# Kernel optimization log

Hardware: AMD Instinct MI355X
Metric: run time of the kernel (lower is better)

## Reference

```python
import math
import jax, jax.numpy as jnp
import numpy as np

# Neuron / simulation constants (from docstring defaults)
THETA = 10.0
TAU_SR = 10.0
TAU_REF = 1.0
SCALE_REF = 2.0
SCALE_RHO = 1.0
TS = 1.0
T_SAMPLE = 300


def _alpha_kernel(tau, mult, eps_tol):
    # Faithful to slayer._calculateAlphaKernel: eps(t) = mult * t/tau * exp(1 - t/tau),
    # truncated once |eps| < eps_tol and t > tau.
    vals = []
    for t in np.arange(0.0, T_SAMPLE, TS):
        v = mult * t / tau * math.exp(1.0 - t / tau)
        if abs(v) < eps_tol and t > tau:
            break
        vals.append(v)
    return np.asarray(vals, np.float32)


def psp(spike, srm_kernel):
    # slayerCuda.conv: causal temporal convolution psp[t] = sum_k f[k] * spike[t-k]
    N, C, H, W, T = spike.shape
    x = spike.reshape(-1, 1, T)                       # (B,1,T), B = N*C*H*W
    K = srm_kernel.shape[0]
    w = jnp.flip(srm_kernel).reshape(1, 1, K).astype(x.dtype)
    y = jax.lax.conv_general_dilated(
        x, w, window_strides=(1,), padding=[(K - 1, 0)],
        dimension_numbers=('NCH', 'OIH', 'NCH'))
    return y.reshape(N, C, H, W, T)


def get_spikes(u2, ref_kernel):
    # slayerCuda.getSpikes: sequential scan over time. At each step the effective
    # membrane potential is u[t] plus pending refractory contributions from past
    # spikes; a spike (value 1/Ts) fires when u_eff >= theta and injects the
    # refractory kernel into future timesteps.
    # u2: (B, T); ref_kernel: (K,) with ref_kernel[0] == 0 (alpha kernel).
    B, T = u2.shape
    K = ref_kernel.shape[0]
    ref_tail = ref_kernel[1:].astype(u2.dtype)        # contributions to t+1..t+K-1

    def step(pend, u_t):
        u_eff = u_t + pend[:, 0]
        s = (u_eff >= THETA).astype(u2.dtype)
        pend = jnp.concatenate([pend[:, 1:], jnp.zeros_like(pend[:, :1])], axis=1)
        pend = pend + s[:, None] * ref_tail[None, :]
        return pend, (s / TS, u_eff)

    pend0 = jnp.zeros((B, K - 1), u2.dtype)
    _, (s, u_mod) = jax.lax.scan(step, pend0, u2.T)
    return s.T, u_mod.T


def setup_inputs() -> dict:
    key = jax.random.key(0)
    k1, = jax.random.split(key, 1)
    N, C, H, W, T = 4, 16, 32, 32, T_SAMPLE
    u = jax.random.uniform(k1, (N, C, H, W, T), dtype=jnp.float32)
    spike_in = (u < 0.05).astype(jnp.float32) / TS
    srm_kernel = jnp.asarray(_alpha_kernel(TAU_SR, 1.0, 0.01))
    ref_kernel = jnp.asarray(_alpha_kernel(TAU_REF, -SCALE_REF * THETA, 0.01))
    return {"spike_in": spike_in, "srm_kernel": srm_kernel, "ref_kernel": ref_kernel}


def reference(spike_in, srm_kernel, ref_kernel):
    # psp (exponential alpha PSP conv) followed by spike generation scan
    u = psp(spike_in, srm_kernel)                     # (N,C,H,W,T)
    T = u.shape[-1]
    s, _ = get_spikes(u.reshape(-1, T), ref_kernel)
    return s.reshape(spike_in.shape)
```

## Files before the change

kernel.cpp:

```cpp
#include <hip/hip_runtime.h>


#define T_LEN 300
#define CH 20
#define NCHUNK 15
#define KS 77
#define KT 76
#define WIN 96
#define KR 10
#define THETA_V 10.0f

__global__ __launch_bounds__(256)
__attribute__((amdgpu_waves_per_eu(1, 1)))
void spike_layer_kernel(
    const float* __restrict__ spike_in,
    const float* __restrict__ srm, int srm_len,
    const float* __restrict__ refk, int ref_len,
    float* __restrict__ out, int B)
{
    int b = blockIdx.x * blockDim.x + threadIdx.x;
    if (b >= B) return;

    const float* row  = spike_in + (size_t)b * T_LEN;
    float*       orow = out      + (size_t)b * T_LEN;

    float srm_r[KS];
#pragma unroll
    for (int i = 1; i < KS; ++i) srm_r[i] = (i < srm_len) ? srm[i] : 0.0f;

    float rt[KR];
#pragma unroll
    for (int i = 0; i < KR; ++i) rt[i] = (i + 1 < ref_len) ? refk[i + 1] : 0.0f;

    float hist[WIN];
#pragma unroll
    for (int i = 0; i < WIN - CH; ++i) hist[i] = 0.0f;

    float pend[KR];
#pragma unroll
    for (int i = 0; i < KR; ++i) pend[i] = 0.0f;

    float nxt[CH];
    {
        const float4* p = (const float4*)row;
#pragma unroll
        for (int i = 0; i < CH / 4; ++i) {
            float4 v = p[i];
            nxt[4*i+0] = v.x; nxt[4*i+1] = v.y; nxt[4*i+2] = v.z; nxt[4*i+3] = v.w;
        }
    }

#pragma unroll 1
    for (int ch = 0; ch < NCHUNK; ++ch) {
#pragma unroll
        for (int i = 0; i < CH; ++i) hist[WIN - CH + i] = nxt[i];

        if (ch + 1 < NCHUNK) {
            const float4* p = (const float4*)(row + (ch + 1) * CH);
#pragma unroll
            for (int i = 0; i < CH / 4; ++i) {
                float4 v = p[i];
                nxt[4*i+0] = v.x; nxt[4*i+1] = v.y; nxt[4*i+2] = v.z; nxt[4*i+3] = v.w;
            }
        }
        __builtin_amdgcn_sched_barrier(0);

        float u[CH];
#pragma unroll
        for (int c = 0; c < CH; ++c) u[c] = 0.0f;
#pragma unroll
        for (int j = 1; j < KS; ++j) {
            const float w = srm_r[j];
#pragma unroll
            for (int c = 0; c < CH; ++c)
                u[c] = fmaf(w, hist[KT + c - j], u[c]);
        }

        float so[CH];
#pragma unroll
        for (int c = 0; c < CH; ++c) {
            const int r = c % KR;
            float u_eff = u[c] + pend[r];
            float s = (u_eff >= THETA_V) ? 1.0f : 0.0f;
#pragma unroll
            for (int i = 0; i < KR - 1; ++i)
                pend[(r + 1 + i) % KR] = fmaf(s, rt[i], pend[(r + 1 + i) % KR]);
            pend[r] = s * rt[KR - 1];
            so[c] = s;
        }

        {
            float4* op = (float4*)(orow + ch * CH);
#pragma unroll
            for (int i = 0; i < CH / 4; ++i) {
                float4 v;
                v.x = so[4*i+0]; v.y = so[4*i+1]; v.z = so[4*i+2]; v.w = so[4*i+3];
                op[i] = v;
            }
        }

#pragma unroll
        for (int i = 0; i < WIN - CH; ++i) hist[i] = hist[i + CH];
    }
}

extern "C" void kernel_launch(void* const* d_in, const int* in_sizes, int n_in,
                              void* d_out, int out_size, void* d_ws, size_t ws_size,
                              hipStream_t stream) {
    const float* spike_in = (const float*)d_in[0];
    const float* srm      = (const float*)d_in[1];
    const float* refk     = (const float*)d_in[2];
    float* out = (float*)d_out;

    int srm_len = in_sizes[1];
    int ref_len = in_sizes[2];
    int B = in_sizes[0] / T_LEN;

    int block = 256;
    int grid = (B + block - 1) / block;
    spike_layer_kernel<<<grid, block, 0, stream>>>(spike_in, srm, srm_len,
                                                   refk, ref_len, out, B);
}
```

Before: 178.4 us.

## Replace dense PSP convolution with sparse spike-bitmask accumulation from shared kernel table

The input history window is now kept as a 96-bit spike bitmask in three registers instead of a 96-float register array. The dense 76-tap FMA convolution is replaced by a wave-uniform loop over set bits. Each set bit adds a shifted slice of the SRM kernel, read from a shared-memory table, into the 20 outputs. This cuts arithmetic and register pressure for sparse inputs. In exchange, it assumes input spikes have unit amplitude, and wave-wide ballot divergence plus LDS bank conflicts depend on spike density.

```diff
diff --git a/kernel.cpp b/kernel.cpp
--- a/kernel.cpp
+++ b/kernel.cpp
@@ -5,10 +5,9 @@
 #define CH 20
 #define NCHUNK 15
 #define KS 77
-#define KT 76
-#define WIN 96
 #define KR 10
 #define THETA_V 10.0f
+#define TSZ 115
 
 __global__ __launch_bounds__(256)
 __attribute__((amdgpu_waves_per_eu(1, 1)))
@@ -18,27 +17,31 @@
     const float* __restrict__ refk, int ref_len,
     float* __restrict__ out, int B)
 {
+    __shared__ float T[TSZ + 13];
+    {
+        int k = threadIdx.x;
+        if (k < TSZ + 13) {
+            int j = k - 19;
+            T[k] = (j >= 1 && j < KS && j < srm_len) ? srm[j] : 0.0f;
+        }
+    }
+    __syncthreads();
+
     int b = blockIdx.x * blockDim.x + threadIdx.x;
     if (b >= B) return;
 
     const float* row  = spike_in + (size_t)b * T_LEN;
     float*       orow = out      + (size_t)b * T_LEN;
 
-    float srm_r[KS];
-#pragma unroll
-    for (int i = 1; i < KS; ++i) srm_r[i] = (i < srm_len) ? srm[i] : 0.0f;
-
     float rt[KR];
 #pragma unroll
     for (int i = 0; i < KR; ++i) rt[i] = (i + 1 < ref_len) ? refk[i + 1] : 0.0f;
 
-    float hist[WIN];
-#pragma unroll
-    for (int i = 0; i < WIN - CH; ++i) hist[i] = 0.0f;
-
     float pend[KR];
 #pragma unroll
     for (int i = 0; i < KR; ++i) pend[i] = 0.0f;
+
+    unsigned w0 = 0, w1 = 0, w2 = 0;
 
     float nxt[CH];
     {
@@ -52,8 +55,14 @@
 
 #pragma unroll 1
     for (int ch = 0; ch < NCHUNK; ++ch) {
+        unsigned nb = 0;
 #pragma unroll
-        for (int i = 0; i < CH; ++i) hist[WIN - CH + i] = nxt[i];
+        for (int i = 0; i < CH; ++i)
+            nb |= (nxt[i] != 0.0f) ? (1u << i) : 0u;
+
+        w0 = (w0 >> 20) | (w1 << 12);
+        w1 = (w1 >> 20) | (w2 << 12);
+        w2 = (w2 >> 20) | (nb << 12);
 
         if (ch + 1 < NCHUNK) {
             const float4* p = (const float4*)(row + (ch + 1) * CH);
@@ -68,12 +77,21 @@
         float u[CH];
 #pragma unroll
         for (int c = 0; c < CH; ++c) u[c] = 0.0f;
-#pragma unroll
-        for (int j = 1; j < KS; ++j) {
-            const float w = srm_r[j];
+
+        unsigned a0 = w0, a1 = w1, a2 = w2;
+        while (__ballot(a0 | a1 | a2)) {
+            int p = a2 ? (95 - __clz(a2))
+                       : (a1 ? (63 - __clz(a1))
+                             : (a0 ? (31 - __clz(a0)) : 95));
+            unsigned m = 1u << (p & 31);
+            if (p >= 64)      a2 &= ~m;
+            else if (p >= 32) a1 &= ~m;
+            else              a0 &= ~m;
+
+            const float* tp = &T[95 - p];
 #pragma unroll
             for (int c = 0; c < CH; ++c)
-                u[c] = fmaf(w, hist[KT + c - j], u[c]);
+                u[c] += tp[c];
         }
 
         float so[CH];
@@ -98,9 +116,6 @@
                 op[i] = v;
             }
         }
-
-#pragma unroll
-        for (int i = 0; i < WIN - CH; ++i) hist[i] = hist[i + CH];
     }
 }
 
```

Result: no change. 179.5 us (+0.6%).
